# Performance work log

Hardware: AMD Instinct MI355X
Metric: run time of the kernel (lower is better)

## Reference

```python
import jax, jax.numpy as jnp
import numpy as np

T, B, IN, H1, HB = 512, 256, 64, 128, 32  # seq, batch, input, LSTM width, bottleneck


def _lstm(x, w_ih, w_hh, b_ih, b_hh):
    """Single-layer unidirectional LSTM, time-major x: [T,B,in] -> [T,B,H].
    PyTorch gate order: i, f, g, o. Zero initial state."""
    H = w_hh.shape[1]
    # hoist input projection out of the scan: [T,B,4H]
    xg = jnp.einsum('tbi,gi->tbg', x, w_ih) + b_ih + b_hh

    def step(carry, xt):
        h, c = carry
        g = xt + h @ w_hh.T
        i, f, gg, o = jnp.split(g, 4, axis=-1)
        c = jax.nn.sigmoid(f) * c + jax.nn.sigmoid(i) * jnp.tanh(gg)
        h = jax.nn.sigmoid(o) * jnp.tanh(c)
        return (h, c), h

    h0 = jnp.zeros((x.shape[1], H), x.dtype)
    (_, _), hs = jax.lax.scan(step, (h0, h0), xg)
    return hs


def setup_inputs() -> dict:
    key = jax.random.key(0)
    ks = jax.random.split(key, 17)
    s = 0.05

    def p(k, shape):
        return jax.random.normal(k, shape, dtype=jnp.float32) * s

    return {
        'X': jax.random.normal(ks[0], (T, B, IN), dtype=jnp.float32),
        # en1: IN -> H1
        'w1_ih': p(ks[1], (4 * H1, IN)), 'w1_hh': p(ks[2], (4 * H1, H1)),
        'b1_ih': p(ks[3], (4 * H1,)), 'b1_hh': p(ks[4], (4 * H1,)),
        # en2: H1 -> HB
        'w2_ih': p(ks[5], (4 * HB, H1)), 'w2_hh': p(ks[6], (4 * HB, HB)),
        'b2_ih': p(ks[7], (4 * HB,)), 'b2_hh': p(ks[8], (4 * HB,)),
        # de1: HB -> H1
        'w3_ih': p(ks[9], (4 * H1, HB)), 'w3_hh': p(ks[10], (4 * H1, H1)),
        'b3_ih': p(ks[11], (4 * H1,)), 'b3_hh': p(ks[12], (4 * H1,)),
        # de2: H1 -> IN
        'w4_ih': p(ks[13], (4 * IN, H1)), 'w4_hh': p(ks[14], (4 * IN, IN)),
        'b4_ih': p(ks[15], (4 * IN,)), 'b4_hh': p(ks[16], (4 * IN,)),
    }


def reference(X, w1_ih, w1_hh, b1_ih, b1_hh, w2_ih, w2_hh, b2_ih, b2_hh,
              w3_ih, w3_hh, b3_ih, b3_hh, w4_ih, w4_hh, b4_ih, b4_hh):
    h = _lstm(X, w1_ih, w1_hh, b1_ih, b1_hh)      # [T,B,128]
    h = _lstm(h, w2_ih, w2_hh, b2_ih, b2_hh)      # [T,B,32]
    h = jnp.tanh(h)                               # bottleneck tanh
    h = _lstm(h, w3_ih, w3_hh, b3_ih, b3_hh)      # [T,B,128]
    out = _lstm(h, w4_ih, w4_hh, b4_ih, b4_hh)    # [T,B,64]
    return out
```

## Files before the change

### kernel.cpp

```cpp
#include <hip/hip_runtime.h>

#define T_STEPS 512
#define BATCH   256

typedef _Float16 f16;
typedef unsigned long long u64;
typedef unsigned int u32;
typedef __attribute__((ext_vector_type(8))) _Float16 f16x8;
typedef __attribute__((ext_vector_type(4))) _Float16 f16x4;
typedef __attribute__((ext_vector_type(4))) float    f32x4;

#define L2E 1.44269504088896340736f

__device__ __forceinline__ float rcp_f(float x)  { return __builtin_amdgcn_rcpf(x); }
__device__ __forceinline__ float exp2_f(float x) { return __builtin_amdgcn_exp2f(x); }

__device__ __forceinline__ float tanh_n(float x) {
    return fmaf(-2.0f, rcp_f(1.0f + exp2_f(2.0f * L2E * x)), 1.0f);
}
__device__ __forceinline__ u64 tanh4_f16(u64 v) {
    f16x4 h = __builtin_bit_cast(f16x4, v);
    f16x4 r;
#pragma unroll
    for (int i = 0; i < 4; ++i) r[i] = (f16)tanh_n((float)h[i]);
    return __builtin_bit_cast(u64, r);
}

__device__ __forceinline__ void barrier_lgkm() {
    asm volatile("s_waitcnt lgkmcnt(0)\n\ts_barrier" ::: "memory");
}
__device__ __forceinline__ void barrier_drain() {
    asm volatile("s_waitcnt vmcnt(0) lgkmcnt(0)\n\ts_barrier" ::: "memory");
}
__device__ __forceinline__ void wait_vm2() {
    asm volatile("s_waitcnt vmcnt(2)" ::: "memory");
}

__device__ __forceinline__ int  flag_load(const int* p) {
    return __hip_atomic_load(p, __ATOMIC_RELAXED, __HIP_MEMORY_SCOPE_AGENT);
}
__device__ __forceinline__ void flag_store(int* p, int v) {
    __hip_atomic_store(p, v, __ATOMIC_RELAXED, __HIP_MEMORY_SCOPE_AGENT);
}
__device__ __forceinline__ u64  panel_load(const u64* p) {
    return __hip_atomic_load(p, __ATOMIC_RELAXED, __HIP_MEMORY_SCOPE_AGENT);
}
__device__ __forceinline__ void panel_store(u64* p, u64 v) {
    __hip_atomic_store(p, v, __ATOMIC_RELAXED, __HIP_MEMORY_SCOPE_AGENT);
}

__device__ __forceinline__ void cvt_store4(f16* dst, f32x4 v) {
    f16x4 h;
    h[0] = (f16)v[0]; h[1] = (f16)v[1]; h[2] = (f16)v[2]; h[3] = (f16)v[3];
    *reinterpret_cast<f16x4*>(dst) = h;
}

template <int IN_DIM, int H>
struct Lstm {
    static constexpr int KTX = IN_DIM / 32, KTH = H / 32, KT = KTX + KTH;
    f16x8 bw[4][KT];
    float bias[4];
    float cst[4];
    int u, q;

    __device__ __forceinline__ void init(const float* __restrict__ w_ih,
                                         const float* __restrict__ w_hh,
                                         const float* __restrict__ b_ih,
                                         const float* __restrict__ b_hh,
                                         int unit, int lane) {
        q = lane >> 4;
        u = unit * 16 + (lane & 15);
#pragma unroll
        for (int g = 0; g < 4; ++g) {
            const float sc = (g == 2) ? 2.0f * L2E : L2E;
            const int row = g * H + u;
#pragma unroll
            for (int kt = 0; kt < KTX; ++kt) {
                const float* p = w_ih + (size_t)row * IN_DIM + kt * 32 + q * 8;
                f16x8 v;
#pragma unroll
                for (int j = 0; j < 8; ++j) v[j] = (f16)(p[j] * sc);
                bw[g][kt] = v;
            }
#pragma unroll
            for (int kt = 0; kt < KTH; ++kt) {
                const float* p = w_hh + (size_t)row * H + kt * 32 + q * 8;
                f16x8 v;
#pragma unroll
                for (int j = 0; j < 8; ++j) v[j] = (f16)(p[j] * sc);
                bw[g][KTX + kt] = v;
            }
            bias[g] = (b_ih[g * H + u] + b_hh[g * H + u]) * sc;
            cst[g] = 0.f;
        }
    }

    __device__ __forceinline__ void step(const f16* in_row, const f16* rec_row,
                                         f16* hdst, int hp, float hold[4]) {
        f16x8 a[KT];
#pragma unroll
        for (int kt = 0; kt < KTX; ++kt)
            a[kt] = *reinterpret_cast<const f16x8*>(in_row + kt * 32 + q * 8);
#pragma unroll
        for (int kt = 0; kt < KTH; ++kt)
            a[KTX + kt] = *reinterpret_cast<const f16x8*>(rec_row + kt * 32 + q * 8);
        f32x4 acc[4];
#pragma unroll
        for (int g = 0; g < 4; ++g)
            acc[g] = (f32x4){bias[g], bias[g], bias[g], bias[g]};
        __builtin_amdgcn_s_setprio(1);
#pragma unroll
        for (int kt = 0; kt < KT; ++kt)
#pragma unroll
            for (int g = 0; g < 4; ++g)
                acc[g] = __builtin_amdgcn_mfma_f32_16x16x32_f16(a[kt], bw[g][kt], acc[g], 0, 0, 0);
#pragma unroll
        for (int r = 0; r < 4; ++r) {
            const float yi = acc[0][r], yf = acc[1][r], yg = acc[2][r], yo = acc[3][r];
            const float Ei = exp2_f(-yi);
            const float G  = exp2_f(yg);
            const float Ef = exp2_f(-yf);
            const float sf = rcp_f(1.0f + Ef);
            const float itg = (2.0f * L2E) * (G - 1.0f) *
                              rcp_f((1.0f + Ei) * (G + 1.0f));
            cst[r] = fmaf(sf, cst[r], itg);
            const float C  = exp2_f(cst[r]);
            const float Eo = exp2_f(-yo);
            const float h  = (C - 1.0f) * rcp_f((1.0f + Eo) * (C + 1.0f));
            hdst[(4 * q + r) * hp + u] = (f16)h;
            hold[r] = h;
        }
        __builtin_amdgcn_s_setprio(0);
    }
};

__global__ __launch_bounds__(768, 3)
void lstm_fused(const float* __restrict__ X,
                const float* __restrict__ w1_ih, const float* __restrict__ w1_hh,
                const float* __restrict__ b1_ih, const float* __restrict__ b1_hh,
                const float* __restrict__ w2_ih, const float* __restrict__ w2_hh,
                const float* __restrict__ b2_ih, const float* __restrict__ b2_hh,
                const float* __restrict__ w3_ih, const float* __restrict__ w3_hh,
                const float* __restrict__ b3_ih, const float* __restrict__ b3_hh,
                const float* __restrict__ w4_ih, const float* __restrict__ w4_hh,
                const float* __restrict__ b4_ih, const float* __restrict__ b4_hh,
                f16* __restrict__ h2t, int* __restrict__ flags,
                float* __restrict__ out)
{
    __shared__ __attribute__((aligned(16))) char sm[16384];
    const int b = blockIdx.x, tid = threadIdx.x;
    const int wave = tid >> 6, lane = tid & 63;
    const int col = lane & 15;

    if (b < 16) {
        const int g = b, bblk = g * 16;
        int* out_flag = flags + g;
        constexpr int XP1 = 72, HP1 = 136, HP2 = 40;
        constexpr int XS_P = 16 * XP1, H1_P = 16 * HP1, H2_P = 16 * HP2;
        f16* xs  = (f16*)sm;
        f16* h1  = (f16*)(sm + 4608);
        f16* h2r = (f16*)(sm + 13312);

        for (int i = tid; i < (2 * H1_P + 2 * H2_P) / 2; i += 768)
            ((u32*)h1)[i] = 0u;

        const float* xg0 = nullptr; const float* xg1 = nullptr;
        f16* xl0 = nullptr; f16* xl1 = nullptr;
        f32x4 hvA0{}, hvA1{}, hvB0{}, hvB1{};
        if (wave >= 10) {
            const int c0 = tid - 640, c1 = c0 + 128;
            const int r0 = c0 >> 4, o0 = (c0 & 15) * 4;
            const int r1 = c1 >> 4, o1 = (c1 & 15) * 4;
            xg0 = X + (size_t)(bblk + r0) * 64 + o0;
            xg1 = X + (size_t)(bblk + r1) * 64 + o1;
            xl0 = xs + r0 * XP1 + o0;
            xl1 = xs + r1 * XP1 + o1;
            f32x4 v0 = *(const f32x4*)xg0, v1 = *(const f32x4*)xg1;
            cvt_store4(xl0, v0); cvt_store4(xl1, v1);
            xg0 += (size_t)BATCH * 64; xg1 += (size_t)BATCH * 64;
            hvA0 = *(const f32x4*)xg0; hvA1 = *(const f32x4*)xg1;
            xg0 += (size_t)BATCH * 64; xg1 += (size_t)BATCH * 64;
            hvB0 = *(const f32x4*)xg0; hvB1 = *(const f32x4*)xg1;
            xg0 += (size_t)BATCH * 64; xg1 += (size_t)BATCH * 64;
        }
        barrier_lgkm();

        if (wave < 8) {
            Lstm<64, 128> L;
            L.init(w1_ih, w1_hh, b1_ih, b1_hh, wave, lane);
            float hd[4];
            const f16* in0 = xs + col * XP1;
            const f16* in1 = xs + XS_P + col * XP1;
            const f16* rc0 = h1 + col * HP1;
            const f16* rc1 = h1 + H1_P + col * HP1;
            f16* d0 = h1;
            f16* d1 = h1 + H1_P;
            for (int ss = 0; ss < 512; ss += 2) {
                L.step(in0, rc1, d0, HP1, hd);
                barrier_lgkm();
                L.step(in1, rc0, d1, HP1, hd);
                barrier_lgkm();
            }
            barrier_lgkm();
            barrier_lgkm();
        } else if (wave < 10) {
            Lstm<128, 32> L;
            L.init(w2_ih, w2_hh, b2_ih, b2_hh, wave - 8, lane);
            float hd[4];
            const int t2id = tid - 512, orow = t2id >> 3, ooff = t2id & 7;
            u64* opg = (u64*)(h2t + (size_t)(bblk + orow) * 32) + ooff;
            const f16* in0 = h1 + col * HP1;
            const f16* in1 = h1 + H1_P + col * HP1;
            const f16* rc0 = h2r + col * HP2;
            const f16* rc1 = h2r + H2_P + col * HP2;
            f16* d0 = h2r;
            f16* d1 = h2r + H2_P;
            const f16* ol0 = h2r + orow * HP2 + ooff * 4;
            const f16* ol1 = h2r + H2_P + orow * HP2 + ooff * 4;
            for (int ss = 0; ss < 512; ss += 2) {
                if (ss >= 2) {
                    panel_store(opg, tanh4_f16(*(const u64*)ol0));
                    opg += (size_t)BATCH * 32 / 4;
                    L.step(in1, rc0, d1, HP2, hd);
                }
                if (ss >= 4 && (ss & 3) == 0) wait_vm2();
                barrier_lgkm();
                if (ss >= 4 && (ss & 3) == 0 && t2id == 0)
                    flag_store(out_flag, ss - 3);
                if (ss >= 2) {
                    panel_store(opg, tanh4_f16(*(const u64*)ol1));
                    opg += (size_t)BATCH * 32 / 4;
                }
                L.step(in0, rc1, d0, HP2, hd);
                barrier_lgkm();
            }
            panel_store(opg, tanh4_f16(*(const u64*)ol0));
            opg += (size_t)BATCH * 32 / 4;
            L.step(in1, rc0, d1, HP2, hd);
            barrier_lgkm();
            panel_store(opg, tanh4_f16(*(const u64*)ol1));
            barrier_drain();
            if (t2id == 0) flag_store(out_flag, T_STEPS + 8);
        } else {
            for (int ss = 0; ss < 512; ss += 2) {
                cvt_store4(xl0 + XS_P, hvA0); cvt_store4(xl1 + XS_P, hvA1);
                if (ss + 3 < 512) {
                    hvA0 = *(const f32x4*)xg0; hvA1 = *(const f32x4*)xg1;
                    xg0 += (size_t)BATCH * 64; xg1 += (size_t)BATCH * 64;
                }
                barrier_lgkm();
                if (ss + 2 < 512) { cvt_store4(xl0, hvB0); cvt_store4(xl1, hvB1); }
                if (ss + 4 < 512) {
                    hvB0 = *(const f32x4*)xg0; hvB1 = *(const f32x4*)xg1;
                    xg0 += (size_t)BATCH * 64; xg1 += (size_t)BATCH * 64;
                }
                barrier_lgkm();
            }
            barrier_lgkm();
            barrier_lgkm();
        }
    } else {
        const int g = b - 16, bblk = g * 16;
        const int* in_flag = flags + g;
        constexpr int XP3 = 40, HP3 = 136, HP4 = 72;
        constexpr int X3_P = 16 * XP3, H3_P = 16 * HP3, H4_P = 16 * HP4;
        f16* xs3 = (f16*)sm;
        f16* h3  = (f16*)(sm + 2560);
        f16* h4  = (f16*)(sm + 11264);

        for (int i = tid; i < (2 * H3_P + 2 * H4_P) / 2; i += 768)
            ((u32*)h3)[i] = 0u;

        const char* sgp = nullptr; f16* slp = nullptr;
        u64 hA0 = 0, hA1 = 0, hB0 = 0, hB1 = 0;
        int seen = 0, flp = 0;
        if (wave == 0) {
            const int r_ = tid >> 2, o_ = (tid & 3) * 8;
            sgp = (const char*)h2t + ((size_t)(bblk + r_) * 32 + o_) * 2;
            slp = xs3 + r_ * XP3 + o_;
            do { seen = flag_load(in_flag); } while (seen < 1);
            u64 pk[2];
            pk[0] = panel_load((const u64*)sgp);
            pk[1] = panel_load((const u64*)sgp + 1);
            sgp += (size_t)BATCH * 64;
            *reinterpret_cast<f16x8*>(slp) = *reinterpret_cast<const f16x8*>(pk);
            while (seen < 2) seen = flag_load(in_flag);
            hA0 = panel_load((const u64*)sgp);
            hA1 = panel_load((const u64*)sgp + 1);
            sgp += (size_t)BATCH * 64;
            while (seen < 3) seen = flag_load(in_flag);
            hB0 = panel_load((const u64*)sgp);
            hB1 = panel_load((const u64*)sgp + 1);
            sgp += (size_t)BATCH * 64;
            flp = seen;
        }
        barrier_lgkm();

        if (wave < 8) {
            Lstm<32, 128> L;
            L.init(w3_ih, w3_hh, b3_ih, b3_hh, wave, lane);
            float hd[4];
            const f16* in0 = xs3 + col * XP3;
            const f16* in1 = xs3 + X3_P + col * XP3;
            const f16* rc0 = h3 + col * HP3;
            const f16* rc1 = h3 + H3_P + col * HP3;
            f16* d0 = h3;
            f16* d1 = h3 + H3_P;
            for (int ss = 0; ss < 512; ss += 2) {
                if (wave == 0) {
                    u64 pk[2] = {hA0, hA1};
                    *reinterpret_cast<f16x8*>(slp + X3_P) = *reinterpret_cast<const f16x8*>(pk);
                    if (ss + 3 < 512) {
                        if (flp > seen) seen = flp;
                        while (seen < ss + 4) seen = flag_load(in_flag);
                        hA0 = panel_load((const u64*)sgp);
                        hA1 = panel_load((const u64*)sgp + 1);
                        sgp += (size_t)BATCH * 64;
                    }
                    flp = flag_load(in_flag);
                }
                L.step(in0, rc1, d0, HP3, hd);
                barrier_lgkm();
                if (wave == 0) {
                    if (ss + 2 < 512) {
                        u64 pk[2] = {hB0, hB1};
                        *reinterpret_cast<f16x8*>(slp) = *reinterpret_cast<const f16x8*>(pk);
                    }
                    if (ss + 4 < 512) {
                        if (flp > seen) seen = flp;
                        while (seen < ss + 5) seen = flag_load(in_flag);
                        hB0 = panel_load((const u64*)sgp);
                        hB1 = panel_load((const u64*)sgp + 1);
                        sgp += (size_t)BATCH * 64;
                    }
                    flp = flag_load(in_flag);
                }
                L.step(in1, rc0, d1, HP3, hd);
                barrier_lgkm();
            }
            barrier_lgkm();
        } else {
            Lstm<128, 64> L;
            L.init(w4_ih, w4_hh, b4_ih, b4_hh, wave - 8, lane);
            float hold[4] = {0.f, 0.f, 0.f, 0.f};
            const int q4 = lane >> 4;
            const int u4 = (wave - 8) * 16 + col;
            float* outp = out + ((size_t)bblk + 4 * q4) * 64 + u4;
            const f16* in0 = h3 + col * HP3;
            const f16* in1 = h3 + H3_P + col * HP3;
            const f16* rc0 = h4 + col * HP4;
            const f16* rc1 = h4 + H4_P + col * HP4;
            f16* d0 = h4;
            f16* d1 = h4 + H4_P;
            for (int ss = 0; ss < 512; ss += 2) {
                if (ss >= 2) {
#pragma unroll
                    for (int r = 0; r < 4; ++r) outp[r * 64] = hold[r];
                    outp += (size_t)BATCH * 64;
                    L.step(in1, rc0, d1, HP4, hold);
                }
                barrier_lgkm();
                if (ss >= 2) {
#pragma unroll
                    for (int r = 0; r < 4; ++r) outp[r * 64] = hold[r];
                    outp += (size_t)BATCH * 64;
                }
                L.step(in0, rc1, d0, HP4, hold);
                barrier_lgkm();
            }
#pragma unroll
            for (int r = 0; r < 4; ++r) outp[r * 64] = hold[r];
            outp += (size_t)BATCH * 64;
            L.step(in1, rc0, d1, HP4, hold);
            barrier_lgkm();
#pragma unroll
            for (int r = 0; r < 4; ++r) outp[r * 64] = hold[r];
        }
    }
}

extern "C" void kernel_launch(void* const* d_in, const int* in_sizes, int n_in,
                              void* d_out, int out_size, void* d_ws, size_t ws_size,
                              hipStream_t stream) {
    const float* X     = (const float*)d_in[0];
    const float* w1_ih = (const float*)d_in[1];
    const float* w1_hh = (const float*)d_in[2];
    const float* b1_ih = (const float*)d_in[3];
    const float* b1_hh = (const float*)d_in[4];
    const float* w2_ih = (const float*)d_in[5];
    const float* w2_hh = (const float*)d_in[6];
    const float* b2_ih = (const float*)d_in[7];
    const float* b2_hh = (const float*)d_in[8];
    const float* w3_ih = (const float*)d_in[9];
    const float* w3_hh = (const float*)d_in[10];
    const float* b3_ih = (const float*)d_in[11];
    const float* b3_hh = (const float*)d_in[12];
    const float* w4_ih = (const float*)d_in[13];
    const float* w4_hh = (const float*)d_in[14];
    const float* b4_ih = (const float*)d_in[15];
    const float* b4_hh = (const float*)d_in[16];

    float* out = (float*)d_out;

    int* flags = (int*)d_ws;
    f16* h2t = (f16*)((char*)d_ws + 256);

    lstm_fused<<<32, 768, 0, stream>>>(X,
        w1_ih, w1_hh, b1_ih, b1_hh, w2_ih, w2_hh, b2_ih, b2_hh,
        w3_ih, w3_hh, b3_ih, b3_hh, w4_ih, w4_hh, b4_ih, b4_hh,
        h2t, flags, out);
}
```

Baseline: 695.8 us.

## Precompute input projections off the recurrent critical path and pre-convert X to fp16

Adds a separate kernel that converts X to fp16 in workspace. The layer-1 and layer-3 waves now load their inputs straight from global memory into registers and run the input-projection MFMAs for the next step right after the current step's gates, so only the recurrent MFMAs sit on the serial dependency chain. The tanh/panel export of layer 2 moves to dedicated waves, and the per-group flag becomes two padded slots read with a min. The cost is an extra kernel launch and extra global traffic, plus a more complex cross-block handshake.

```diff
diff --git a/kernel.cpp b/kernel.cpp
--- a/kernel.cpp
+++ b/kernel.cpp
@@ -29,12 +29,12 @@
 __device__ __forceinline__ void barrier_lgkm() {
     asm volatile("s_waitcnt lgkmcnt(0)\n\ts_barrier" ::: "memory");
 }
-__device__ __forceinline__ void barrier_drain() {
-    asm volatile("s_waitcnt vmcnt(0) lgkmcnt(0)\n\ts_barrier" ::: "memory");
-}
 __device__ __forceinline__ void wait_vm2() {
     asm volatile("s_waitcnt vmcnt(2)" ::: "memory");
 }
+__device__ __forceinline__ void wait_vm0() {
+    asm volatile("s_waitcnt vmcnt(0)" ::: "memory");
+}
 
 __device__ __forceinline__ int  flag_load(const int* p) {
     return __hip_atomic_load(p, __ATOMIC_RELAXED, __HIP_MEMORY_SCOPE_AGENT);
@@ -48,11 +48,9 @@
 __device__ __forceinline__ void panel_store(u64* p, u64 v) {
     __hip_atomic_store(p, v, __ATOMIC_RELAXED, __HIP_MEMORY_SCOPE_AGENT);
 }
-
-__device__ __forceinline__ void cvt_store4(f16* dst, f32x4 v) {
-    f16x4 h;
-    h[0] = (f16)v[0]; h[1] = (f16)v[1]; h[2] = (f16)v[2]; h[3] = (f16)v[3];
-    *reinterpret_cast<f16x4*>(dst) = h;
+__device__ __forceinline__ int flag_min2(const int* p) {
+    const int a = flag_load(p), b = flag_load(p + 1);
+    return a < b ? a : b;
 }
 
 template <int IN_DIM, int H>
@@ -95,25 +93,31 @@
         }
     }
 
-    __device__ __forceinline__ void step(const f16* in_row, const f16* rec_row,
-                                         f16* hdst, int hp, float hold[4]) {
-        f16x8 a[KT];
-#pragma unroll
-        for (int kt = 0; kt < KTX; ++kt)
-            a[kt] = *reinterpret_cast<const f16x8*>(in_row + kt * 32 + q * 8);
-#pragma unroll
-        for (int kt = 0; kt < KTH; ++kt)
-            a[KTX + kt] = *reinterpret_cast<const f16x8*>(rec_row + kt * 32 + q * 8);
-        f32x4 acc[4];
+    __device__ __forceinline__ void acc_init(f32x4 acc[4]) const {
 #pragma unroll
         for (int g = 0; g < 4; ++g)
             acc[g] = (f32x4){bias[g], bias[g], bias[g], bias[g]};
-        __builtin_amdgcn_s_setprio(1);
-#pragma unroll
-        for (int kt = 0; kt < KT; ++kt)
-#pragma unroll
-            for (int g = 0; g < 4; ++g)
-                acc[g] = __builtin_amdgcn_mfma_f32_16x16x32_f16(a[kt], bw[g][kt], acc[g], 0, 0, 0);
+    }
+    __device__ __forceinline__ void mfma_kt(f32x4 acc[4], f16x8 a, int kt) const {
+#pragma unroll
+        for (int g = 0; g < 4; ++g)
+            acc[g] = __builtin_amdgcn_mfma_f32_16x16x32_f16(a, bw[g][kt], acc[g], 0, 0, 0);
+    }
+    __device__ __forceinline__ void mfma_in(f32x4 acc[4], const f16* in_row) const {
+#pragma unroll
+        for (int kt = 0; kt < KTX; ++kt) {
+            f16x8 a = *reinterpret_cast<const f16x8*>(in_row + kt * 32 + q * 8);
+            mfma_kt(acc, a, kt);
+        }
+    }
+    __device__ __forceinline__ void mfma_rec(f32x4 acc[4], const f16* rec_row) const {
+#pragma unroll
+        for (int kt = 0; kt < KTH; ++kt) {
+            f16x8 a = *reinterpret_cast<const f16x8*>(rec_row + kt * 32 + q * 8);
+            mfma_kt(acc, a, KTX + kt);
+        }
+    }
+    __device__ __forceinline__ void gates(f32x4 acc[4], f16* hdst, int hp, float hold[4]) {
 #pragma unroll
         for (int r = 0; r < 4; ++r) {
             const float yi = acc[0][r], yf = acc[1][r], yg = acc[2][r], yo = acc[3][r];
@@ -130,12 +134,22 @@
             hdst[(4 * q + r) * hp + u] = (f16)h;
             hold[r] = h;
         }
-        __builtin_amdgcn_s_setprio(0);
     }
 };
 
+__global__ __launch_bounds__(256)
+void cvt_x(const float* __restrict__ X, f16* __restrict__ xh) {
+    const size_t i = ((size_t)blockIdx.x * 256 + threadIdx.x) * 8;
+    const f32x4 a = *reinterpret_cast<const f32x4*>(X + i);
+    const f32x4 b = *reinterpret_cast<const f32x4*>(X + i + 4);
+    f16x8 o;
+    o[0] = (f16)a[0]; o[1] = (f16)a[1]; o[2] = (f16)a[2]; o[3] = (f16)a[3];
+    o[4] = (f16)b[0]; o[5] = (f16)b[1]; o[6] = (f16)b[2]; o[7] = (f16)b[3];
+    *reinterpret_cast<f16x8*>(xh + i) = o;
+}
+
 __global__ __launch_bounds__(768, 3)
-void lstm_fused(const float* __restrict__ X,
+void lstm_fused(const f16* __restrict__ xh,
                 const float* __restrict__ w1_ih, const float* __restrict__ w1_hh,
                 const float* __restrict__ b1_ih, const float* __restrict__ b1_hh,
                 const float* __restrict__ w2_ih, const float* __restrict__ w2_hh,
@@ -150,229 +164,186 @@
     __shared__ __attribute__((aligned(16))) char sm[16384];
     const int b = blockIdx.x, tid = threadIdx.x;
     const int wave = tid >> 6, lane = tid & 63;
-    const int col = lane & 15;
+    const int col = lane & 15, q = lane >> 4;
 
     if (b < 16) {
         const int g = b, bblk = g * 16;
-        int* out_flag = flags + g;
-        constexpr int XP1 = 72, HP1 = 136, HP2 = 40;
-        constexpr int XS_P = 16 * XP1, H1_P = 16 * HP1, H2_P = 16 * HP2;
-        f16* xs  = (f16*)sm;
-        f16* h1  = (f16*)(sm + 4608);
-        f16* h2r = (f16*)(sm + 13312);
+        int* out_flag = flags + g * 32;
+        constexpr int HP1 = 136, HP2 = 40;
+        constexpr int H1_P = 16 * HP1, H2_P = 16 * HP2;
+        f16* h1  = (f16*)sm;
+        f16* h2r = (f16*)(sm + 8704);
 
         for (int i = tid; i < (2 * H1_P + 2 * H2_P) / 2; i += 768)
             ((u32*)h1)[i] = 0u;
-
-        const float* xg0 = nullptr; const float* xg1 = nullptr;
-        f16* xl0 = nullptr; f16* xl1 = nullptr;
-        f32x4 hvA0{}, hvA1{}, hvB0{}, hvB1{};
-        if (wave >= 10) {
-            const int c0 = tid - 640, c1 = c0 + 128;
-            const int r0 = c0 >> 4, o0 = (c0 & 15) * 4;
-            const int r1 = c1 >> 4, o1 = (c1 & 15) * 4;
-            xg0 = X + (size_t)(bblk + r0) * 64 + o0;
-            xg1 = X + (size_t)(bblk + r1) * 64 + o1;
-            xl0 = xs + r0 * XP1 + o0;
-            xl1 = xs + r1 * XP1 + o1;
-            f32x4 v0 = *(const f32x4*)xg0, v1 = *(const f32x4*)xg1;
-            cvt_store4(xl0, v0); cvt_store4(xl1, v1);
-            xg0 += (size_t)BATCH * 64; xg1 += (size_t)BATCH * 64;
-            hvA0 = *(const f32x4*)xg0; hvA1 = *(const f32x4*)xg1;
-            xg0 += (size_t)BATCH * 64; xg1 += (size_t)BATCH * 64;
-            hvB0 = *(const f32x4*)xg0; hvB1 = *(const f32x4*)xg1;
-            xg0 += (size_t)BATCH * 64; xg1 += (size_t)BATCH * 64;
-        }
-        barrier_lgkm();
 
         if (wave < 8) {
             Lstm<64, 128> L;
             L.init(w1_ih, w1_hh, b1_ih, b1_hh, wave, lane);
             float hd[4];
-            const f16* in0 = xs + col * XP1;
-            const f16* in1 = xs + XS_P + col * XP1;
-            const f16* rc0 = h1 + col * HP1;
-            const f16* rc1 = h1 + H1_P + col * HP1;
-            f16* d0 = h1;
-            f16* d1 = h1 + H1_P;
-            for (int ss = 0; ss < 512; ss += 2) {
-                L.step(in0, rc1, d0, HP1, hd);
-                barrier_lgkm();
-                L.step(in1, rc0, d1, HP1, hd);
-                barrier_lgkm();
-            }
-            barrier_lgkm();
-            barrier_lgkm();
+            const size_t xstep = (size_t)BATCH * 64;
+            const f16* xg = xh + (size_t)(bblk + col) * 64 + q * 8;
+            f32x4 accA[4], accB[4];
+            f16x8 xfE[2], xfO[2];
+            {
+                f16x8 t0 = *reinterpret_cast<const f16x8*>(xg);
+                f16x8 t1 = *reinterpret_cast<const f16x8*>(xg + 32);
+                L.acc_init(accA);
+                L.mfma_kt(accA, t0, 0);
+                L.mfma_kt(accA, t1, 1);
+                xfO[0] = *reinterpret_cast<const f16x8*>(xg + 1 * xstep);
+                xfO[1] = *reinterpret_cast<const f16x8*>(xg + 1 * xstep + 32);
+                xfE[0] = *reinterpret_cast<const f16x8*>(xg + 2 * xstep);
+                xfE[1] = *reinterpret_cast<const f16x8*>(xg + 2 * xstep + 32);
+            }
+            barrier_lgkm();
+            auto sub = [&](int par, int s, f32x4 accCur[4], f32x4 accNext[4],
+                           f16x8 xf[2]) {
+                if (s < 512) {
+                    __builtin_amdgcn_s_setprio(1);
+                    L.mfma_rec(accCur, h1 + (par ^ 1) * H1_P + col * HP1);
+                    L.gates(accCur, h1 + par * H1_P, HP1, hd);
+                    __builtin_amdgcn_s_setprio(0);
+                    L.acc_init(accNext);
+                    L.mfma_kt(accNext, xf[0], 0);
+                    L.mfma_kt(accNext, xf[1], 1);
+                    if (s + 3 < 512) {
+                        const f16* p = xg + (size_t)(s + 3) * xstep;
+                        xf[0] = *reinterpret_cast<const f16x8*>(p);
+                        xf[1] = *reinterpret_cast<const f16x8*>(p + 32);
+                    }
+                }
+                barrier_lgkm();
+            };
+            for (int ss = 0; ss < 514; ss += 2) {
+                sub(0, ss,     accA, accB, xfO);
+                sub(1, ss + 1, accB, accA, xfE);
+            }
         } else if (wave < 10) {
             Lstm<128, 32> L;
             L.init(w2_ih, w2_hh, b2_ih, b2_hh, wave - 8, lane);
             float hd[4];
-            const int t2id = tid - 512, orow = t2id >> 3, ooff = t2id & 7;
-            u64* opg = (u64*)(h2t + (size_t)(bblk + orow) * 32) + ooff;
-            const f16* in0 = h1 + col * HP1;
-            const f16* in1 = h1 + H1_P + col * HP1;
-            const f16* rc0 = h2r + col * HP2;
-            const f16* rc1 = h2r + H2_P + col * HP2;
-            f16* d0 = h2r;
-            f16* d1 = h2r + H2_P;
-            const f16* ol0 = h2r + orow * HP2 + ooff * 4;
-            const f16* ol1 = h2r + H2_P + orow * HP2 + ooff * 4;
-            for (int ss = 0; ss < 512; ss += 2) {
-                if (ss >= 2) {
-                    panel_store(opg, tanh4_f16(*(const u64*)ol0));
-                    opg += (size_t)BATCH * 32 / 4;
-                    L.step(in1, rc0, d1, HP2, hd);
-                }
-                if (ss >= 4 && (ss & 3) == 0) wait_vm2();
-                barrier_lgkm();
-                if (ss >= 4 && (ss & 3) == 0 && t2id == 0)
-                    flag_store(out_flag, ss - 3);
-                if (ss >= 2) {
-                    panel_store(opg, tanh4_f16(*(const u64*)ol1));
-                    opg += (size_t)BATCH * 32 / 4;
-                }
-                L.step(in0, rc1, d0, HP2, hd);
-                barrier_lgkm();
-            }
-            panel_store(opg, tanh4_f16(*(const u64*)ol0));
-            opg += (size_t)BATCH * 32 / 4;
-            L.step(in1, rc0, d1, HP2, hd);
-            barrier_lgkm();
-            panel_store(opg, tanh4_f16(*(const u64*)ol1));
-            barrier_drain();
-            if (t2id == 0) flag_store(out_flag, T_STEPS + 8);
+            barrier_lgkm();
+            auto sub = [&](int par, int s) {
+                if (s >= 1 && s <= 512) {
+                    __builtin_amdgcn_s_setprio(1);
+                    f32x4 acc[4];
+                    L.acc_init(acc);
+                    L.mfma_in(acc, h1 + (par ^ 1) * H1_P + col * HP1);
+                    L.mfma_rec(acc, h2r + par * H2_P + col * HP2);
+                    L.gates(acc, h2r + (par ^ 1) * H2_P, HP2, hd);
+                    __builtin_amdgcn_s_setprio(0);
+                }
+                barrier_lgkm();
+            };
+            for (int ss = 0; ss < 514; ss += 2) { sub(0, ss); sub(1, ss + 1); }
         } else {
-            for (int ss = 0; ss < 512; ss += 2) {
-                cvt_store4(xl0 + XS_P, hvA0); cvt_store4(xl1 + XS_P, hvA1);
-                if (ss + 3 < 512) {
-                    hvA0 = *(const f32x4*)xg0; hvA1 = *(const f32x4*)xg1;
-                    xg0 += (size_t)BATCH * 64; xg1 += (size_t)BATCH * 64;
-                }
-                barrier_lgkm();
-                if (ss + 2 < 512) { cvt_store4(xl0, hvB0); cvt_store4(xl1, hvB1); }
-                if (ss + 4 < 512) {
-                    hvB0 = *(const f32x4*)xg0; hvB1 = *(const f32x4*)xg1;
-                    xg0 += (size_t)BATCH * 64; xg1 += (size_t)BATCH * 64;
-                }
-                barrier_lgkm();
-            }
-            barrier_lgkm();
-            barrier_lgkm();
+            const int pb = tid - 640, prow = pb >> 3, poff = pb & 7;
+            int* slot = out_flag + (pb >> 6);
+            const u64* pl0 = (const u64*)(h2r + prow * HP2 + poff * 4);
+            const u64* pl1 = (const u64*)(h2r + H2_P + prow * HP2 + poff * 4);
+            u64* opg = (u64*)(h2t + (size_t)(bblk + prow) * 32) + poff;
+            constexpr size_t pstep = (size_t)BATCH * 32 / 4;
+            barrier_lgkm();
+            auto sub = [&](int par, int s, const u64* src) {
+                if (s >= 2 && s <= 513) {
+                    const int p = s - 2;
+                    panel_store(opg + (size_t)p * pstep, tanh4_f16(*src));
+                    if (s >= 6 && (s & 3) == 2) {
+                        wait_vm2();
+                        if ((pb & 63) == 0) flag_store(slot, s - 3);
+                    }
+                }
+                barrier_lgkm();
+            };
+            for (int ss = 0; ss < 514; ss += 2) { sub(0, ss, pl0); sub(1, ss + 1, pl1); }
+            wait_vm0();
+            if ((pb & 63) == 0) flag_store(slot, 1 << 20);
         }
     } else {
         const int g = b - 16, bblk = g * 16;
-        const int* in_flag = flags + g;
-        constexpr int XP3 = 40, HP3 = 136, HP4 = 72;
-        constexpr int X3_P = 16 * XP3, H3_P = 16 * HP3, H4_P = 16 * HP4;
-        f16* xs3 = (f16*)sm;
-        f16* h3  = (f16*)(sm + 2560);
-        f16* h4  = (f16*)(sm + 11264);
+        const int* in_flag = flags + g * 32;
+        constexpr int HP3 = 136, HP4 = 72;
+        constexpr int H3_P = 16 * HP3, H4_P = 16 * HP4;
+        f16* h3 = (f16*)sm;
+        f16* h4 = (f16*)(sm + 8704);
 
         for (int i = tid; i < (2 * H3_P + 2 * H4_P) / 2; i += 768)
             ((u32*)h3)[i] = 0u;
-
-        const char* sgp = nullptr; f16* slp = nullptr;
-        u64 hA0 = 0, hA1 = 0, hB0 = 0, hB1 = 0;
-        int seen = 0, flp = 0;
-        if (wave == 0) {
-            const int r_ = tid >> 2, o_ = (tid & 3) * 8;
-            sgp = (const char*)h2t + ((size_t)(bblk + r_) * 32 + o_) * 2;
-            slp = xs3 + r_ * XP3 + o_;
-            do { seen = flag_load(in_flag); } while (seen < 1);
-            u64 pk[2];
-            pk[0] = panel_load((const u64*)sgp);
-            pk[1] = panel_load((const u64*)sgp + 1);
-            sgp += (size_t)BATCH * 64;
-            *reinterpret_cast<f16x8*>(slp) = *reinterpret_cast<const f16x8*>(pk);
-            while (seen < 2) seen = flag_load(in_flag);
-            hA0 = panel_load((const u64*)sgp);
-            hA1 = panel_load((const u64*)sgp + 1);
-            sgp += (size_t)BATCH * 64;
-            while (seen < 3) seen = flag_load(in_flag);
-            hB0 = panel_load((const u64*)sgp);
-            hB1 = panel_load((const u64*)sgp + 1);
-            sgp += (size_t)BATCH * 64;
-            flp = seen;
-        }
-        barrier_lgkm();
 
         if (wave < 8) {
             Lstm<32, 128> L;
             L.init(w3_ih, w3_hh, b3_ih, b3_hh, wave, lane);
             float hd[4];
-            const f16* in0 = xs3 + col * XP3;
-            const f16* in1 = xs3 + X3_P + col * XP3;
-            const f16* rc0 = h3 + col * HP3;
-            const f16* rc1 = h3 + H3_P + col * HP3;
-            f16* d0 = h3;
-            f16* d1 = h3 + H3_P;
-            for (int ss = 0; ss < 512; ss += 2) {
-                if (wave == 0) {
-                    u64 pk[2] = {hA0, hA1};
-                    *reinterpret_cast<f16x8*>(slp + X3_P) = *reinterpret_cast<const f16x8*>(pk);
-                    if (ss + 3 < 512) {
-                        if (flp > seen) seen = flp;
-                        while (seen < ss + 4) seen = flag_load(in_flag);
-                        hA0 = panel_load((const u64*)sgp);
-                        hA1 = panel_load((const u64*)sgp + 1);
-                        sgp += (size_t)BATCH * 64;
+            const u64* pg = (const u64*)h2t + (size_t)(bblk + col) * 8 + q * 2;
+            constexpr size_t pstep = (size_t)BATCH * 8;
+            f32x4 accA[4], accB[4];
+            u64 xE[2], xO[2];
+            int fl = -1, flp = -1;
+            {
+                do { fl = flag_min2(in_flag); } while (fl < 1);
+                u64 t0 = panel_load(pg), t1 = panel_load(pg + 1);
+                u64 pk[2] = {t0, t1};
+                L.acc_init(accA);
+                L.mfma_kt(accA, *reinterpret_cast<const f16x8*>(pk), 0);
+                while (fl < 2) fl = flag_min2(in_flag);
+                xO[0] = panel_load(pg + 1 * pstep);
+                xO[1] = panel_load(pg + 1 * pstep + 1);
+                while (fl < 3) fl = flag_min2(in_flag);
+                xE[0] = panel_load(pg + 2 * pstep);
+                xE[1] = panel_load(pg + 2 * pstep + 1);
+                flp = flag_min2(in_flag);
+            }
+            barrier_lgkm();
+            auto sub = [&](int par, int t, f32x4 accCur[4], f32x4 accNext[4],
+                           u64 xf[2]) {
+                if (t < 512) {
+                    __builtin_amdgcn_s_setprio(1);
+                    L.mfma_rec(accCur, h3 + (par ^ 1) * H3_P + col * HP3);
+                    L.gates(accCur, h3 + par * H3_P, HP3, hd);
+                    __builtin_amdgcn_s_setprio(0);
+                    L.acc_init(accNext);
+                    u64 pk[2] = {xf[0], xf[1]};
+                    L.mfma_kt(accNext, *reinterpret_cast<const f16x8*>(pk), 0);
+                    if (t + 3 < 512) {
+                        if (flp > fl) fl = flp;
+                        while (fl < t + 4) fl = flag_min2(in_flag);
+                        const u64* p = pg + (size_t)(t + 3) * pstep;
+                        xf[0] = panel_load(p);
+                        xf[1] = panel_load(p + 1);
+                        flp = flag_min2(in_flag);
                     }
-                    flp = flag_load(in_flag);
-                }
-                L.step(in0, rc1, d0, HP3, hd);
-                barrier_lgkm();
-                if (wave == 0) {
-                    if (ss + 2 < 512) {
-                        u64 pk[2] = {hB0, hB1};
-                        *reinterpret_cast<f16x8*>(slp) = *reinterpret_cast<const f16x8*>(pk);
-                    }
-                    if (ss + 4 < 512) {
-                        if (flp > seen) seen = flp;
-                        while (seen < ss + 5) seen = flag_load(in_flag);
-                        hB0 = panel_load((const u64*)sgp);
-                        hB1 = panel_load((const u64*)sgp + 1);
-                        sgp += (size_t)BATCH * 64;
-                    }
-                    flp = flag_load(in_flag);
-                }
-                L.step(in1, rc0, d1, HP3, hd);
-                barrier_lgkm();
-            }
-            barrier_lgkm();
+                }
+                barrier_lgkm();
+            };
+            for (int tt = 0; tt < 514; tt += 2) {
+                sub(0, tt,     accA, accB, xO);
+                sub(1, tt + 1, accB, accA, xE);
+            }
         } else {
             Lstm<128, 64> L;
             L.init(w4_ih, w4_hh, b4_ih, b4_hh, wave - 8, lane);
             float hold[4] = {0.f, 0.f, 0.f, 0.f};
-            const int q4 = lane >> 4;
-            const int u4 = (wave - 8) * 16 + col;
-            float* outp = out + ((size_t)bblk + 4 * q4) * 64 + u4;
-            const f16* in0 = h3 + col * HP3;
-            const f16* in1 = h3 + H3_P + col * HP3;
-            const f16* rc0 = h4 + col * HP4;
-            const f16* rc1 = h4 + H4_P + col * HP4;
-            f16* d0 = h4;
-            f16* d1 = h4 + H4_P;
-            for (int ss = 0; ss < 512; ss += 2) {
-                if (ss >= 2) {
-#pragma unroll
-                    for (int r = 0; r < 4; ++r) outp[r * 64] = hold[r];
-                    outp += (size_t)BATCH * 64;
-                    L.step(in1, rc0, d1, HP4, hold);
-                }
-                barrier_lgkm();
-                if (ss >= 2) {
-#pragma unroll
-                    for (int r = 0; r < 4; ++r) outp[r * 64] = hold[r];
-                    outp += (size_t)BATCH * 64;
-                }
-                L.step(in0, rc1, d0, HP4, hold);
-                barrier_lgkm();
-            }
-#pragma unroll
-            for (int r = 0; r < 4; ++r) outp[r * 64] = hold[r];
-            outp += (size_t)BATCH * 64;
-            L.step(in1, rc0, d1, HP4, hold);
-            barrier_lgkm();
+            float* outp = out + ((size_t)bblk + 4 * q) * 64 + (wave - 8) * 16 + col;
+            barrier_lgkm();
+            auto sub = [&](int par, int t) {
+                if (t >= 1 && t <= 512) {
+                    if (t >= 2) {
+#pragma unroll
+                        for (int r = 0; r < 4; ++r) outp[r * 64] = hold[r];
+                        outp += (size_t)BATCH * 64;
+                    }
+                    __builtin_amdgcn_s_setprio(1);
+                    f32x4 acc[4];
+                    L.acc_init(acc);
+                    L.mfma_in(acc, h3 + (par ^ 1) * H3_P + col * HP3);
+                    L.mfma_rec(acc, h4 + par * H4_P + col * HP4);
+                    L.gates(acc, h4 + (par ^ 1) * H4_P, HP4, hold);
+                    __builtin_amdgcn_s_setprio(0);
+                }
+                barrier_lgkm();
+            };
+            for (int tt = 0; tt < 514; tt += 2) { sub(0, tt); sub(1, tt + 1); }
 #pragma unroll
             for (int r = 0; r < 4; ++r) outp[r * 64] = hold[r];
         }
@@ -403,9 +374,11 @@
     float* out = (float*)d_out;
 
     int* flags = (int*)d_ws;
-    f16* h2t = (f16*)((char*)d_ws + 256);
-
-    lstm_fused<<<32, 768, 0, stream>>>(X,
+    f16* h2t = (f16*)((char*)d_ws + 4096);
+    f16* xh  = (f16*)((char*)d_ws + 4096 + (size_t)T_STEPS * BATCH * 32 * 2);
+
+    cvt_x<<<4096, 256, 0, stream>>>(X, xh);
+    lstm_fused<<<32, 768, 0, stream>>>(xh,
         w1_ih, w1_hh, b1_ih, b1_hh, w2_ih, w2_hh, b2_ih, b2_hh,
         w3_ih, w3_hh, b3_ih, b3_hh, w4_ih, w4_hh, b4_ih, b4_hh,
         h2t, flags, out);
```

Measured after the change: 862.6 us. +24.0%, slower.
